# Optimization experiments

Measured on AMD Instinct MI355X. Metric: run time of the kernel, lower is better.

Reference implementation:

```python
import jax, jax.numpy as jnp
import numpy as np

B, S, D = 16, 4096, 64
SCALE = float(np.sqrt(D))  # sqrt(hidden_size)


def setup_inputs() -> dict:
    key = jax.random.key(0)
    kq, kk, kv = jax.random.split(key, 3)
    return {
        "query": jax.random.normal(kq, (B, S, D), dtype=jnp.float32),
        "key": jax.random.normal(kk, (B, S, D), dtype=jnp.float32),
        "value": jax.random.normal(kv, (B, S, D), dtype=jnp.float32),
    }


def reference(query, key, value):
    # energy: [B, S, S]
    energy = jnp.einsum("bqd,bkd->bqk", query, key) / SCALE
    attention = jax.nn.softmax(energy, axis=2)
    return jnp.einsum("bqk,bkd->bqd", attention, value)
```

## Files before the change

kernel.cpp:

```cpp
#include <hip/hip_runtime.h>


#define NBATCH 16
#define SEQ    4096
#define DIM    64
#define BQ     256
#define BK     64
#define NKT    (SEQ / BK)
#define KHALF  (NKT / 2)
#define OELEMS (NBATCH * SEQ * DIM)
#define NROWS  (NBATCH * SEQ)
#define NTILES (NBATCH * NKT)
#define TILEH  4096

#define QSCALE 0.180336879f

typedef _Float16 half2_t __attribute__((ext_vector_type(2)));
typedef _Float16 half4_t __attribute__((ext_vector_type(4)));
typedef _Float16 half8_t __attribute__((ext_vector_type(8)));
typedef float    floatx4 __attribute__((ext_vector_type(4)));

__device__ inline float fast_exp2(float x) {
#if __has_builtin(__builtin_amdgcn_exp2f)
  return __builtin_amdgcn_exp2f(x);
#else
  return exp2f(x);
#endif
}
__device__ inline float fast_rcp(float x) {
#if __has_builtin(__builtin_amdgcn_rcpf)
  return __builtin_amdgcn_rcpf(x);
#else
  return 1.0f / x;
#endif
}

__device__ inline int swz(int row, int col) {
  return row * 64 + ((((col >> 3) ^ ((row >> 1) & 7)) << 3) | (col & 7));
}

__device__ inline void async16(const void* g, void* l) {
  __builtin_amdgcn_global_load_lds(
      (const __attribute__((address_space(1))) void*)g,
      (__attribute__((address_space(3))) void*)l, 16, 0, 0);
}

__global__ __launch_bounds__(256, 2)
void prepack_kv(const float* __restrict__ Kg, const float* __restrict__ Vg,
                _Float16* __restrict__ Kh, _Float16* __restrict__ Vh)
{
  __shared__ __align__(16) _Float16 sKi[TILEH];
  __shared__ __align__(16) _Float16 sVi[TILEH];
  const int tid = threadIdx.x;
  const int t16 = tid & 15;
  const int kg  = tid >> 4;
  const int bt  = blockIdx.x;
  const float* Kt_ = Kg + (size_t)bt * BK * DIM;
  const float* Vt_ = Vg + (size_t)bt * BK * DIM;

  floatx4 kbuf[4], vbuf[4];
  #pragma unroll
  for (int i = 0; i < 4; ++i) {
    const int key = kg + 16 * i;
    kbuf[i] = *(const floatx4*)(Kt_ + key * DIM + t16 * 4);
    vbuf[i] = *(const floatx4*)(Vt_ + key * DIM + t16 * 4);
  }
  #pragma unroll
  for (int i = 0; i < 4; ++i) {
    const int key = kg + 16 * i;
    half4_t h;
    #pragma unroll
    for (int j = 0; j < 4; ++j) h[j] = (_Float16)kbuf[i][j];
    *(half4_t*)&sKi[swz(key, t16 * 4)] = h;
  }
  {
    const int vbase = (kg >> 2) * 8 + (kg & 3) * 2;
    #pragma unroll
    for (int e = 0; e < 4; ++e) {
      const int dim = t16 * 4 + e;
      half2_t h0; h0[0] = (_Float16)vbuf[0][e]; h0[1] = (_Float16)vbuf[1][e];
      half2_t h1; h1[0] = (_Float16)vbuf[2][e]; h1[1] = (_Float16)vbuf[3][e];
      *(half2_t*)&sVi[swz(dim, vbase)]      = h0;
      *(half2_t*)&sVi[swz(dim, vbase + 32)] = h1;
    }
  }
  __syncthreads();
  half8_t* Ko = (half8_t*)(Kh + (size_t)bt * TILEH);
  half8_t* Vo = (half8_t*)(Vh + (size_t)bt * TILEH);
  const half8_t* Ks = (const half8_t*)sKi;
  const half8_t* Vs = (const half8_t*)sVi;
  Ko[tid] = Ks[tid]; Ko[tid + 256] = Ks[tid + 256];
  Vo[tid] = Vs[tid]; Vo[tid + 256] = Vs[tid + 256];
}

__global__ __launch_bounds__(256, 2)
void attn_f16_flash(const float* __restrict__ Qg, const _Float16* __restrict__ Kh,
                    const _Float16* __restrict__ Vh, float* __restrict__ O0g,
                    float* __restrict__ O1g, float* __restrict__ lsg)
{
  __shared__ __align__(16) _Float16 sT[4][2 * TILEH];

  const int tid  = threadIdx.x;
  const int wave = tid >> 6;
  const int lane = tid & 63;
  const int l16  = lane & 15;
  const int quad = lane >> 4;
  const int hK   = (l16 >> 1) & 7;

  const int bid  = blockIdx.x;
  const int x    = bid & 7;
  const int r    = bid >> 3;
  const int b    = x + ((r & 1) << 3);
  const int qt   = (r >> 1) & 15;
  const int half = (r >> 5) & 1;
  const int q0   = qt * BQ + wave * 64;
  const int kt0  = half * KHALF;

  const float* Qb = Qg + ((size_t)b * SEQ + q0) * DIM;
  float*       Ob = (half ? O1g : O0g) + ((size_t)b * SEQ + q0) * DIM;
  float*       Ls = lsg + (size_t)half * NROWS + b * SEQ + q0;

  half8_t qf[4][2];
  #pragma unroll
  for (int s = 0; s < 4; ++s)
    #pragma unroll
    for (int c = 0; c < 2; ++c) {
      const floatx4 f0 = *(const floatx4*)(Qb + (s * 16 + l16) * DIM + c * 32 + quad * 8);
      const floatx4 f1 = *(const floatx4*)(Qb + (s * 16 + l16) * DIM + c * 32 + quad * 8 + 4);
      half8_t h;
      #pragma unroll
      for (int j = 0; j < 4; ++j) h[j] = (_Float16)(f0[j] * QSCALE);
      #pragma unroll
      for (int j = 0; j < 4; ++j) h[4 + j] = (_Float16)(f1[j] * QSCALE);
      qf[s][c] = h;
    }

  floatx4 oacc2[4][4];
  float   lsum2[4];
  #pragma unroll
  for (int n = 0; n < 4; ++n)
    #pragma unroll
    for (int s = 0; s < 4; ++s) oacc2[n][s] = (floatx4){0.f, 0.f, 0.f, 0.f};
  #pragma unroll
  for (int s = 0; s < 4; ++s) lsum2[s] = 0.f;

  #define ASYNC(KT, BUF)                                                       \
    do {                                                                       \
      const char* gk = (const char*)(Kh + ((size_t)b * NKT + (KT)) * TILEH)    \
                       + wave * 2048;                                          \
      const char* gv = (const char*)(Vh + ((size_t)b * NKT + (KT)) * TILEH)    \
                       + wave * 2048;                                          \
      char* lk = (char*)(&sT[BUF][0])     + wave * 2048;                       \
      char* lv = (char*)(&sT[BUF][TILEH]) + wave * 2048;                       \
      async16(gk + lane * 16,        lk);                                      \
      async16(gk + 1024 + lane * 16, lk + 1024);                               \
      async16(gv + lane * 16,        lv);                                      \
      async16(gv + 1024 + lane * 16, lv + 1024);                               \
    } while (0)

  #define COMPUTE(BUF)                                                         \
    do {                                                                       \
      const _Float16* SKB = &sT[BUF][0];                                       \
      const _Float16* SVB = &sT[BUF][TILEH];                                   \
      _Pragma("unroll")                                                        \
      for (int h = 0; h < 2; ++h) {                                            \
        floatx4 sc2[2][4];                                                     \
        _Pragma("unroll")                                                      \
        for (int k2 = 0; k2 < 2; ++k2)                                         \
          _Pragma("unroll")                                                    \
          for (int s = 0; s < 4; ++s) sc2[k2][s] = (floatx4){0.f, 0.f, 0.f, 0.f};\
        __builtin_amdgcn_s_setprio(1);                                         \
        _Pragma("unroll")                                                      \
        for (int k2 = 0; k2 < 2; ++k2) {                                       \
          const int nk = h * 2 + k2;                                           \
          _Pragma("unroll")                                                    \
          for (int c = 0; c < 2; ++c) {                                        \
            half8_t kf = *(const half8_t*)&SKB[(nk * 16 + l16) * 64 +          \
                                               (((c * 4 + quad) ^ hK) << 3)];  \
            _Pragma("unroll")                                                  \
            for (int s = 0; s < 4; ++s)                                        \
              sc2[k2][s] = __builtin_amdgcn_mfma_f32_16x16x32_f16(             \
                  kf, qf[s][c], sc2[k2][s], 0, 0, 0);                          \
          }                                                                    \
        }                                                                      \
        __builtin_amdgcn_s_setprio(0);                                         \
        half8_t bfr[4];                                                        \
        _Pragma("unroll")                                                      \
        for (int s = 0; s < 4; ++s) {                                          \
          half8_t bf;                                                          \
          _Pragma("unroll")                                                    \
          for (int j = 0; j < 8; ++j) {                                        \
            float p = fast_exp2(sc2[j & 1][s][j >> 1]);                        \
            lsum2[s] += p;                                                     \
            bf[j] = (_Float16)p;                                               \
          }                                                                    \
          bfr[s] = bf;                                                         \
        }                                                                      \
        __builtin_amdgcn_s_setprio(1);                                         \
        _Pragma("unroll")                                                      \
        for (int n = 0; n < 4; ++n) {                                          \
          half8_t vf = *(const half8_t*)&SVB[(n * 16 + l16) * 64 +             \
                                             (((h * 4 + quad) ^ hK) << 3)];    \
          _Pragma("unroll")                                                    \
          for (int s = 0; s < 4; ++s)                                          \
            oacc2[n][s] = __builtin_amdgcn_mfma_f32_16x16x32_f16(              \
                vf, bfr[s], oacc2[n][s], 0, 0, 0);                             \
        }                                                                      \
        __builtin_amdgcn_s_setprio(0);                                         \
      }                                                                        \
    } while (0)

  #define GATE(N)                                                              \
    do {                                                                       \
      asm volatile("s_waitcnt vmcnt(" #N ")" ::: "memory");                    \
      __builtin_amdgcn_s_barrier();                                            \
      __builtin_amdgcn_sched_barrier(0);                                       \
    } while (0)

  ASYNC(kt0 + 0, 0);
  ASYNC(kt0 + 1, 1);

  #pragma unroll 1
  for (int t = 0; t < KHALF - 2; ++t) {
    GATE(4);
    ASYNC(kt0 + t + 2, (t + 2) & 3);
    COMPUTE(t & 3);
  }
  GATE(4);
  COMPUTE((KHALF - 2) & 3);
  GATE(0);
  COMPUTE((KHALF - 1) & 3);

  #pragma unroll
  for (int s = 0; s < 4; ++s) {
    float v = lsum2[s];
    v += __shfl_xor(v, 16);
    v += __shfl_xor(v, 32);
    if (lane < 16) Ls[s * 16 + l16] = v;
  }
  #pragma unroll
  for (int s = 0; s < 4; ++s)
    #pragma unroll
    for (int n = 0; n < 4; ++n)
      *(floatx4*)&Ob[(s * 16 + l16) * DIM + n * 16 + quad * 4] = oacc2[n][s];

  #undef ASYNC
  #undef COMPUTE
  #undef GATE
}

__global__ __launch_bounds__(256)
void attn_combine(float* __restrict__ O, const float* __restrict__ O1,
                  const float* __restrict__ lsg)
{
  const int i = blockIdx.x * 256 + threadIdx.x;
  const int row = i >> 4;
  const float inv = fast_rcp(lsg[row] + lsg[NROWS + row]);
  const float4 a  = ((const float4*)O)[i];
  const float4 bb = ((const float4*)O1)[i];
  float4 r;
  r.x = (a.x + bb.x) * inv;
  r.y = (a.y + bb.y) * inv;
  r.z = (a.z + bb.z) * inv;
  r.w = (a.w + bb.w) * inv;
  ((float4*)O)[i] = r;
}

extern "C" void kernel_launch(void* const* d_in, const int* in_sizes, int n_in,
                              void* d_out, int out_size, void* d_ws, size_t ws_size,
                              hipStream_t stream) {
  const float* Q = (const float*)d_in[0];
  const float* K = (const float*)d_in[1];
  const float* V = (const float*)d_in[2];
  float* O  = (float*)d_out;
  (void)in_sizes; (void)n_in; (void)out_size; (void)ws_size;

  float*     O1 = (float*)d_ws;
  float*     Ls = O1 + OELEMS;
  _Float16*  Kh = (_Float16*)(Ls + 2 * NROWS);
  _Float16*  Vh = Kh + (size_t)NTILES * TILEH;

  prepack_kv<<<dim3(NTILES), dim3(256), 0, stream>>>(K, V, Kh, Vh);
  attn_f16_flash<<<dim3(2 * NBATCH * (SEQ / BQ)), dim3(256), 0, stream>>>(
      Q, Kh, Vh, O, O1, Ls);
  attn_combine<<<dim3(OELEMS / 4 / 256), dim3(256), 0, stream>>>(O, O1, Ls);
}
```

Measured before the change: 163.6 us.

## Software-pipeline QK, exp and PV across half-tiles to overlap MFMA with exp

Splits the per-tile compute into QK, exponent and PV stages on half-tiles and interleaves them. The next half's QK MFMAs are issued before the current half's exp and PV work, so matrix-core work overlaps the transcendental VALU work. It also removes the s_setprio hints and moves the async prefetch gate into the middle of each iteration. In exchange it keeps two sets of score and fp16 probability registers live at once, which raises register pressure and may reduce occupancy.

New measurement: 164.9 us. About the same (+0.8%).

```diff
diff --git a/kernel.cpp b/kernel.cpp
--- a/kernel.cpp
+++ b/kernel.cpp
@@ -158,55 +158,54 @@
       async16(gv + 1024 + lane * 16, lv + 1024);                               \
     } while (0)
 
-  #define COMPUTE(BUF)                                                         \
+  #define QKH(scX, BUF, H)                                                     \
     do {                                                                       \
       const _Float16* SKB = &sT[BUF][0];                                       \
+      _Pragma("unroll")                                                        \
+      for (int k2 = 0; k2 < 2; ++k2)                                           \
+        _Pragma("unroll")                                                      \
+        for (int s = 0; s < 4; ++s) scX[k2][s] = (floatx4){0.f, 0.f, 0.f, 0.f};\
+      _Pragma("unroll")                                                        \
+      for (int k2 = 0; k2 < 2; ++k2) {                                         \
+        const int nk = (H) * 2 + k2;                                           \
+        _Pragma("unroll")                                                      \
+        for (int c = 0; c < 2; ++c) {                                          \
+          half8_t kf = *(const half8_t*)&SKB[(nk * 16 + l16) * 64 +            \
+                                             (((c * 4 + quad) ^ hK) << 3)];    \
+          _Pragma("unroll")                                                    \
+          for (int s = 0; s < 4; ++s)                                          \
+            scX[k2][s] = __builtin_amdgcn_mfma_f32_16x16x32_f16(               \
+                kf, qf[s][c], scX[k2][s], 0, 0, 0);                            \
+        }                                                                      \
+      }                                                                        \
+    } while (0)
+
+  #define EXPH(scX, bfrX)                                                      \
+    do {                                                                       \
+      _Pragma("unroll")                                                        \
+      for (int s = 0; s < 4; ++s) {                                            \
+        half8_t bf;                                                            \
+        _Pragma("unroll")                                                      \
+        for (int j = 0; j < 8; ++j) {                                          \
+          float p = fast_exp2(scX[j & 1][s][j >> 1]);                          \
+          lsum2[s] += p;                                                       \
+          bf[j] = (_Float16)p;                                                 \
+        }                                                                      \
+        bfrX[s] = bf;                                                          \
+      }                                                                        \
+    } while (0)
+
+  #define PVH(bfrX, BUF, H)                                                    \
+    do {                                                                       \
       const _Float16* SVB = &sT[BUF][TILEH];                                   \
       _Pragma("unroll")                                                        \
-      for (int h = 0; h < 2; ++h) {                                            \
-        floatx4 sc2[2][4];                                                     \
+      for (int n = 0; n < 4; ++n) {                                            \
+        half8_t vf = *(const half8_t*)&SVB[(n * 16 + l16) * 64 +               \
+                                           ((((H) * 4 + quad) ^ hK) << 3)];    \
         _Pragma("unroll")                                                      \
-        for (int k2 = 0; k2 < 2; ++k2)                                         \
-          _Pragma("unroll")                                                    \
-          for (int s = 0; s < 4; ++s) sc2[k2][s] = (floatx4){0.f, 0.f, 0.f, 0.f};\
-        __builtin_amdgcn_s_setprio(1);                                         \
-        _Pragma("unroll")                                                      \
-        for (int k2 = 0; k2 < 2; ++k2) {                                       \
-          const int nk = h * 2 + k2;                                           \
-          _Pragma("unroll")                                                    \
-          for (int c = 0; c < 2; ++c) {                                        \
-            half8_t kf = *(const half8_t*)&SKB[(nk * 16 + l16) * 64 +          \
-                                               (((c * 4 + quad) ^ hK) << 3)];  \
-            _Pragma("unroll")                                                  \
-            for (int s = 0; s < 4; ++s)                                        \
-              sc2[k2][s] = __builtin_amdgcn_mfma_f32_16x16x32_f16(             \
-                  kf, qf[s][c], sc2[k2][s], 0, 0, 0);                          \
-          }                                                                    \
-        }                                                                      \
-        __builtin_amdgcn_s_setprio(0);                                         \
-        half8_t bfr[4];                                                        \
-        _Pragma("unroll")                                                      \
-        for (int s = 0; s < 4; ++s) {                                          \
-          half8_t bf;                                                          \
-          _Pragma("unroll")                                                    \
-          for (int j = 0; j < 8; ++j) {                                        \
-            float p = fast_exp2(sc2[j & 1][s][j >> 1]);                        \
-            lsum2[s] += p;                                                     \
-            bf[j] = (_Float16)p;                                               \
-          }                                                                    \
-          bfr[s] = bf;                                                         \
-        }                                                                      \
-        __builtin_amdgcn_s_setprio(1);                                         \
-        _Pragma("unroll")                                                      \
-        for (int n = 0; n < 4; ++n) {                                          \
-          half8_t vf = *(const half8_t*)&SVB[(n * 16 + l16) * 64 +             \
-                                             (((h * 4 + quad) ^ hK) << 3)];    \
-          _Pragma("unroll")                                                    \
-          for (int s = 0; s < 4; ++s)                                          \
-            oacc2[n][s] = __builtin_amdgcn_mfma_f32_16x16x32_f16(              \
-                vf, bfr[s], oacc2[n][s], 0, 0, 0);                             \
-        }                                                                      \
-        __builtin_amdgcn_s_setprio(0);                                         \
+        for (int s = 0; s < 4; ++s)                                            \
+          oacc2[n][s] = __builtin_amdgcn_mfma_f32_16x16x32_f16(                \
+              vf, bfrX[s], oacc2[n][s], 0, 0, 0);                              \
       }                                                                        \
     } while (0)
 
@@ -217,19 +216,46 @@
       __builtin_amdgcn_sched_barrier(0);                                       \
     } while (0)
 
+  floatx4 scA[2][4], scB[2][4];
+  half8_t bfrA[4], bfrB[4];
+
   ASYNC(kt0 + 0, 0);
   ASYNC(kt0 + 1, 1);
+  GATE(4);
+  ASYNC(kt0 + 2, 2);
+  QKH(scA, 0, 0);
 
   #pragma unroll 1
   for (int t = 0; t < KHALF - 2; ++t) {
+    const int cb = t & 3;
+    QKH(scB, cb, 1);
+    EXPH(scA, bfrA);
+    PVH(bfrA, cb, 0);
     GATE(4);
-    ASYNC(kt0 + t + 2, (t + 2) & 3);
-    COMPUTE(t & 3);
-  }
-  GATE(4);
-  COMPUTE((KHALF - 2) & 3);
-  GATE(0);
-  COMPUTE((KHALF - 1) & 3);
+    if (t + 3 < KHALF) ASYNC(kt0 + t + 3, (t + 3) & 3);
+    QKH(scA, (t + 1) & 3, 0);
+    EXPH(scB, bfrB);
+    PVH(bfrB, cb, 1);
+  }
+
+  {
+    const int cb = (KHALF - 2) & 3;
+    QKH(scB, cb, 1);
+    EXPH(scA, bfrA);
+    PVH(bfrA, cb, 0);
+    GATE(0);
+    QKH(scA, (KHALF - 1) & 3, 0);
+    EXPH(scB, bfrB);
+    PVH(bfrB, cb, 1);
+  }
+  {
+    const int cb = (KHALF - 1) & 3;
+    QKH(scB, cb, 1);
+    EXPH(scA, bfrA);
+    PVH(bfrA, cb, 0);
+    EXPH(scB, bfrB);
+    PVH(bfrB, cb, 1);
+  }
 
   #pragma unroll
   for (int s = 0; s < 4; ++s) {
@@ -245,7 +271,9 @@
       *(floatx4*)&Ob[(s * 16 + l16) * DIM + n * 16 + quad * 4] = oacc2[n][s];
 
   #undef ASYNC
-  #undef COMPUTE
+  #undef QKH
+  #undef EXPH
+  #undef PVH
   #undef GATE
 }
 
```
